# Performance work log

Hardware: AMD Instinct MI355X
Metric: run time of the kernel (lower is better)

The kernel has to match this reference:

```python
import jax, jax.numpy as jnp
import numpy as np

B, V, H, W, CIN, COUT = 2, 4, 256, 256, 64, 64
WINDOW = 1
GAMMA = 0.1


def setup_inputs() -> dict:
    key = jax.random.key(0)
    ks = jax.random.split(key, 6)
    # gaussian positions: x,y in [-1,1], z in [0.5,2.5] so projection masks are nontrivial
    means = jax.random.uniform(ks[0], (B, V, H, W, 3), dtype=jnp.float32)
    means = means * jnp.array([2.0, 2.0, 2.0], jnp.float32) + jnp.array([-1.0, -1.0, 0.5], jnp.float32)
    depths = jax.random.uniform(ks[1], (B, V, H, W, 1, 1), dtype=jnp.float32)
    gs_feats = jax.random.normal(ks[2], (B, V, H, W, CIN), dtype=jnp.float32)
    # normalized intrinsics (ndc in [0,1))
    intr = jnp.array([[0.8, 0.0, 0.5], [0.0, 0.8, 0.5], [0.0, 0.0, 1.0]], jnp.float32)
    intrinsics = jnp.broadcast_to(intr, (B, V, 3, 3))
    # camera-to-world extrinsics: identity rotation, small per-view translations
    t = jax.random.uniform(ks[3], (B, V, 3), minval=-0.2, maxval=0.2, dtype=jnp.float32)
    extrinsics = jnp.broadcast_to(jnp.eye(4, dtype=jnp.float32), (B, V, 4, 4)).at[..., :3, 3].set(t)
    w1 = jax.random.normal(ks[4], (COUT, CIN, 3, 3), dtype=jnp.float32) * 0.05
    b1 = jnp.zeros((COUT,), jnp.float32)
    w2 = jax.random.normal(ks[5], (COUT, COUT, 3, 3), dtype=jnp.float32) * 0.05
    b2 = jnp.zeros((COUT,), jnp.float32)
    return {"means": means, "depths": depths, "gs_feats": gs_feats,
            "intrinsics": intrinsics, "extrinsics": extrinsics,
            "w1": w1, "b1": b1, "w2": w2, "b2": b2}


def _project(points, intr, extr, eps=1e-8):
    # points (b, n, 3) world; extr (b,4,4) cam-to-world; intr (b,3,3) normalized
    w2c = jnp.linalg.inv(extr)
    ph = jnp.concatenate([points, jnp.ones_like(points[..., :1])], axis=-1)  # (b,n,4)
    cam = jnp.einsum('bij,bnj->bni', w2c, ph)[..., :3]
    z = cam[..., 2:3]
    ndc = jnp.einsum('bij,bnj->bni', intr, cam / (z + eps))
    return ndc[..., :2], cam[..., 2] > eps


def _conv3x3(x, w, b):
    y = jax.lax.conv_general_dilated(x, w, (1, 1), 'SAME',
                                     dimension_numbers=('NCHW', 'OIHW', 'NCHW'))
    return y + b[None, :, None, None]


def reference(means, depths, gs_feats, intrinsics, extrinsics, w1, b1, w2, b2):
    b, v, h, w_, c = gs_feats.shape
    hw = h * w_
    feats_flat = gs_feats.reshape(b, v, hw, c)
    pts = means.reshape(b, v, hw, 3)
    outs = []
    for j in range(v):
        acc = feats_flat[:, j]                      # (b, hw, c)
        norm = jnp.ones((b,), gs_feats.dtype)
        for k in range(v):
            if j != k and (k - WINDOW) <= j <= (k + WINDOW):
                ndc, valid_z = _project(pts[:, j], intrinsics[:, k], extrinsics[:, k])
                px = jnp.floor(ndc[..., 0] * w_).astype(jnp.int32)
                py = jnp.floor(ndc[..., 1] * h).astype(jnp.int32)
                mask = ((ndc[..., 0] >= 0) & (ndc[..., 0] < 1) &
                        (ndc[..., 1] >= 0) & (ndc[..., 1] < 1) & valid_z)  # (b,hw)
                idx = jnp.clip(py, 0, h - 1) * w_ + jnp.clip(px, 0, w_ - 1)
                gathered = jnp.take_along_axis(feats_flat[:, k], idx[..., None], axis=1)
                upd = jnp.where(mask[..., None], gathered, jnp.zeros((), gs_feats.dtype))
                scale = GAMMA * mask.sum(-1).astype(gs_feats.dtype) / (h * w_)  # (b,)
                acc = acc + upd * scale[:, None, None]
                norm = norm + scale
        outs.append(acc / norm[:, None, None])
    fused = jnp.stack(outs, axis=1).reshape(b * v, h, w_, c).transpose(0, 3, 1, 2)  # (bv,c,h,w)
    x = _conv3x3(fused, w1, b1)
    x = jax.nn.gelu(x, approximate=False)
    x = _conv3x3(x, w2, b2)
    return x.transpose(0, 2, 3, 1).reshape(b, v, h, w_, -1)
```

## Files before the change

kernel.cpp:

```cpp
#include <hip/hip_runtime.h>
#include <math.h>

#define HW 65536
#define NPAD 258

typedef short bf16x8 __attribute__((ext_vector_type(8)));
typedef float f32x4  __attribute__((ext_vector_type(4)));

#define O_COUNTS 0
#define O_W2C    2048
#define O_WT     4096
#define O_META   151552
#define O_FUSED  3297280
#define O_X1     71458816

#define ROWPX 66
#define ROWB  (ROWPX * 128)
#define ROWSTR (ROWB + 16)
#define ROWSTRS (ROWSTR / 2)

__device__ __forceinline__ unsigned short f2bf(float f) {
    unsigned int u = __float_as_uint(f);
    u += 0x7FFFu + ((u >> 16) & 1u);
    return (unsigned short)(u >> 16);
}

__global__ __launch_bounds__(256) void prep_kernel(
    const float* __restrict__ extr, const float* __restrict__ w1,
    const float* __restrict__ w2, float* __restrict__ w2c,
    unsigned short* __restrict__ wT, unsigned short* __restrict__ fusedP,
    unsigned short* __restrict__ x1P, int* __restrict__ counts)
{
    int tid = blockIdx.x * blockDim.x + threadIdx.x;
    int nth = gridDim.x * blockDim.x;

    if (blockIdx.x == 0) {
        if (threadIdx.x < 8) {
            float a[4][8];
            const float* E = extr + threadIdx.x * 16;
            for (int r = 0; r < 4; r++)
                for (int c = 0; c < 4; c++) {
                    a[r][c] = E[r*4 + c];
                    a[r][4+c] = (r == c) ? 1.0f : 0.0f;
                }
            for (int col = 0; col < 4; col++) {
                int piv = col; float bm = fabsf(a[col][col]);
                for (int r = col+1; r < 4; r++) {
                    float v = fabsf(a[r][col]);
                    if (v > bm) { bm = v; piv = r; }
                }
                if (piv != col)
                    for (int c = 0; c < 8; c++) { float t = a[col][c]; a[col][c] = a[piv][c]; a[piv][c] = t; }
                float f = 1.0f / a[col][col];
                for (int c = 0; c < 8; c++) a[col][c] *= f;
                for (int r = 0; r < 4; r++) if (r != col) {
                    float f2 = a[r][col];
                    for (int c = 0; c < 8; c++) a[r][c] -= f2 * a[col][c];
                }
            }
            float* O = w2c + threadIdx.x * 16;
            for (int r = 0; r < 4; r++)
                for (int c = 0; c < 4; c++) O[r*4+c] = a[r][4+c];
        }
    }

    for (int i = tid; i < 384; i += nth) counts[i] = 0;

    for (int e = tid; e < 73728; e += nth) {
        int t = e;
        int j  = t & 7;  t >>= 3;
        int co = t & 63; t >>= 6;
        int q  = t & 3;  t >>= 2;
        int tap = t % 9; t /= 9;
        int h  = t & 1;  int cv = t >> 1;
        int ci = h*32 + q*8 + j;
        int ky = tap / 3, kx = tap % 3;
        const float* wsrc = cv ? w2 : w1;
        float v = wsrc[((co*64 + ci)*3 + ky)*3 + kx];
        wT[cv*36864 + ((((h*9 + tap)*4 + q)*64 + co)*8 + j)] = f2bf(v);
    }

    for (int u = tid; u < 2*8*1028*8; u += nth) {
        int t = u;
        int ch   = t & 7;    t >>= 3;
        int cell = t % 1028; t /= 1028;
        int n    = t & 7;    int buf = t >> 3;
        int y, x;
        if      (cell < 258) { y = 0;   x = cell; }
        else if (cell < 516) { y = 257; x = cell - 258; }
        else if (cell < 772) { y = cell - 516 + 1; x = 0; }
        else                 { y = cell - 772 + 1; x = 257; }
        unsigned short* p = (buf ? x1P : fusedP) +
            (((size_t)(n*NPAD + y)*NPAD + x)*64 + ch*8);
        *reinterpret_cast<uint4*>(p) = make_uint4(0u, 0u, 0u, 0u);
    }
}

__global__ __launch_bounds__(256) void proj_kernel(
    const float* __restrict__ means, const float* __restrict__ intr,
    const float* __restrict__ w2c, int* __restrict__ meta,
    int* __restrict__ counts)
{
    const int jt[6] = {0,1,1,2,2,3};
    const int kt[6] = {1,0,2,1,3,2};
    int s = blockIdx.y;
    int b = s / 6, p = s % 6;
    int j = jt[p], k = kt[p];
    int i = blockIdx.x * 256 + threadIdx.x;

    __shared__ int bcnt;
    if (threadIdx.x == 0) bcnt = 0;
    __syncthreads();

    const float* mp = means + ((size_t)(b*4 + j)*HW + i)*3;
    float x = mp[0], y = mp[1], z = mp[2];
    const float* M = w2c + (b*4 + k)*16;
    const float* I = intr + (b*4 + k)*9;

    float cx = fmaf(M[2],  z, fmaf(M[1], y, M[0]*x)) + M[3];
    float cy = fmaf(M[6],  z, fmaf(M[5], y, M[4]*x)) + M[7];
    float cz = fmaf(M[10], z, fmaf(M[9], y, M[8]*x)) + M[11];

    bool vz = cz > 1e-8f;
    float zi = cz + 1e-8f;
    float sx = cx / zi, sy = cy / zi, sz = cz / zi;
    float nx = fmaf(I[2], sz, fmaf(I[1], sy, I[0]*sx));
    float ny = fmaf(I[5], sz, fmaf(I[4], sy, I[3]*sx));

    int px = (int)floorf(nx * 256.0f);
    int py = (int)floorf(ny * 256.0f);
    bool mask = (nx >= 0.0f) && (nx < 1.0f) && (ny >= 0.0f) && (ny < 1.0f) && vz;
    int pxc = min(max(px, 0), 255);
    int pyc = min(max(py, 0), 255);
    int idx = pyc*256 + pxc;
    meta[(size_t)s*HW + i] = idx | (mask ? (int)0x80000000 : 0);

    unsigned long long bal = __ballot(mask ? 1 : 0);
    if ((threadIdx.x & 63) == 0)
        atomicAdd(&bcnt, (int)__popcll(bal));
    __syncthreads();
    if (threadIdx.x == 0)
        atomicAdd(counts + s*32, bcnt);
}

__global__ __launch_bounds__(256) void fuse_kernel(
    const float* __restrict__ feats, const int* __restrict__ meta,
    const int* __restrict__ counts, unsigned short* __restrict__ fusedP)
{
    const int nsl[4]    = {1, 2, 2, 1};
    const int slt[4][2] = {{0,0},{1,2},{3,4},{5,5}};
    const int kvw[4][2] = {{1,1},{0,2},{1,3},{2,2}};

    int bj = blockIdx.y;
    int b = bj >> 2, j = bj & 3;
    int pt = blockIdx.x * 16 + (threadIdx.x >> 4);
    int cg = threadIdx.x & 15;

    const float4* fj = reinterpret_cast<const float4*>(
        feats + ((size_t)bj*HW + pt)*64) + cg;
    float4 acc = *fj;
    float norm = 1.0f;
    int ns = nsl[j];
    for (int e = 0; e < 2; e++) {
        if (e < ns) {
            int p = slt[j][e], k = kvw[j][e];
            int s = b*6 + p;
            float scale = 0.1f * (float)counts[s*32] / 65536.0f;
            int mt = meta[(size_t)s*HW + pt];
            if (mt < 0) {
                int idx = mt & 0xFFFF;
                const float4* g = reinterpret_cast<const float4*>(
                    feats + ((size_t)(b*4 + k)*HW + idx)*64) + cg;
                float4 gv = *g;
                acc.x += scale * gv.x; acc.y += scale * gv.y;
                acc.z += scale * gv.z; acc.w += scale * gv.w;
            }
            norm += scale;
        }
    }
    float ox = acc.x / norm, oy = acc.y / norm;
    float oz = acc.z / norm, ow = acc.w / norm;

    int yy = pt >> 8, xx = pt & 255;
    unsigned short* op = fusedP +
        (((size_t)bj*NPAD + (yy+1))*NPAD + (xx+1))*64 + cg*4;
    ushort4 o = make_ushort4(f2bf(ox), f2bf(oy), f2bf(oz), f2bf(ow));
    *reinterpret_cast<ushort4*>(op) = o;
}

template<int MODE>
__global__ __launch_bounds__(256) void conv_kernel(
    const unsigned short* __restrict__ in, const unsigned short* __restrict__ wT,
    const float* __restrict__ bias, void* __restrict__ outp)
{
    __shared__ unsigned short smem[6 * ROWSTRS];

    int n = blockIdx.z;
    int y0 = blockIdx.y * 4;
    int X0 = blockIdx.x * 64;
    int w  = threadIdx.x >> 6;
    int lane = threadIdx.x & 63;
    int m = lane & 15, q = lane >> 4;

    for (int ri = w; ri < 6; ri += 4) {
        const char* g = (const char*)(in + ((size_t)(n*NPAD + y0 + ri)*NPAD + X0)*64);
        char* l = (char*)smem + ri*ROWSTR;
#pragma unroll
        for (int i = 0; i < 8; i++)
            __builtin_amdgcn_global_load_lds(
                (const __attribute__((address_space(1))) unsigned int*)(g + i*1024 + (size_t)lane*16),
                (__attribute__((address_space(3))) unsigned int*)(l + i*1024 + (size_t)lane*16),
                16, 0, 0);
        __builtin_amdgcn_global_load_lds(
            (const __attribute__((address_space(1))) unsigned int*)(g + 8192 + (size_t)lane*4),
            (__attribute__((address_space(3))) unsigned int*)(l + 8192 + (size_t)lane*4),
            4, 0, 0);
    }
    __syncthreads();

    f32x4 acc[4][4];
#pragma unroll
    for (int a = 0; a < 4; a++)
#pragma unroll
        for (int bq = 0; bq < 4; bq++)
            acc[a][bq] = (f32x4){0.f, 0.f, 0.f, 0.f};

#pragma unroll
    for (int h = 0; h < 2; h++) {
#pragma unroll
        for (int tap = 0; tap < 9; tap++) {
            int dy = tap/3, dx = tap%3;
            const unsigned short* lrow = smem + (w + dy)*ROWSTRS;
            bf16x8 av[4], bv[4];
#pragma unroll
            for (int Mt = 0; Mt < 4; Mt++)
                av[Mt] = *reinterpret_cast<const bf16x8*>(
                    lrow + (Mt*16 + m + dx)*64 + h*32 + q*8);
            const unsigned short* wp = wT + (size_t)(((h*9 + tap)*4 + q)*64)*8;
#pragma unroll
            for (int Nt = 0; Nt < 4; Nt++)
                bv[Nt] = *reinterpret_cast<const bf16x8*>(wp + (Nt*16 + m)*8);
#pragma unroll
            for (int Mt = 0; Mt < 4; Mt++)
#pragma unroll
                for (int Nt = 0; Nt < 4; Nt++)
                    acc[Mt][Nt] = __builtin_amdgcn_mfma_f32_16x16x32_bf16(
                        av[Mt], bv[Nt], acc[Mt][Nt], 0, 0, 0);
        }
    }

#pragma unroll
    for (int Nt = 0; Nt < 4; Nt++) {
        int co = Nt*16 + m;
        float bs = bias[co];
#pragma unroll
        for (int Mt = 0; Mt < 4; Mt++) {
#pragma unroll
            for (int r = 0; r < 4; r++) {
                float v = acc[Mt][Nt][r] + bs;
                int px = X0 + Mt*16 + q*4 + r;
                if (MODE == 1) {
                    v = 0.5f * v * (1.0f + erff(v * 0.70710678118654752f));
                    unsigned short* o = (unsigned short*)outp +
                        ((size_t)(n*NPAD + y0 + w + 1)*NPAD + (px + 1))*64 + co;
                    *o = f2bf(v);
                } else {
                    float* o = (float*)outp +
                        ((size_t)(n*256 + y0 + w)*256 + px)*64 + co;
                    *o = v;
                }
            }
        }
    }
}

extern "C" void kernel_launch(void* const* d_in, const int* in_sizes, int n_in,
                              void* d_out, int out_size, void* d_ws, size_t ws_size,
                              hipStream_t stream)
{
    const float* means = (const float*)d_in[0];
    const float* feats = (const float*)d_in[2];
    const float* intr  = (const float*)d_in[3];
    const float* extr  = (const float*)d_in[4];
    const float* w1    = (const float*)d_in[5];
    const float* b1    = (const float*)d_in[6];
    const float* w2    = (const float*)d_in[7];
    const float* b2    = (const float*)d_in[8];

    char* ws = (char*)d_ws;
    int*            counts = (int*)(ws + O_COUNTS);
    float*          w2c    = (float*)(ws + O_W2C);
    unsigned short* wT     = (unsigned short*)(ws + O_WT);
    int*            meta   = (int*)(ws + O_META);
    unsigned short* fusedP = (unsigned short*)(ws + O_FUSED);
    unsigned short* x1P    = (unsigned short*)(ws + O_X1);

    prep_kernel<<<dim3(96), dim3(256), 0, stream>>>(
        extr, w1, w2, w2c, wT, fusedP, x1P, counts);
    proj_kernel<<<dim3(256, 12), dim3(256), 0, stream>>>(
        means, intr, w2c, meta, counts);
    fuse_kernel<<<dim3(4096, 8), dim3(256), 0, stream>>>(
        feats, meta, counts, fusedP);
    conv_kernel<1><<<dim3(4, 64, 8), dim3(256), 0, stream>>>(
        fusedP, wT, b1, (void*)x1P);
    conv_kernel<2><<<dim3(4, 64, 8), dim3(256), 0, stream>>>(
        x1P, wT + 36864, b2, d_out);
}
```

Before: 417.5 us.

## Swizzle conv LDS tile layout and vectorize epilogue stores via swapped MFMA operands

Conv input rows are now staged into LDS with an XOR swizzle on the 16-byte channel chunks, and the A-fragment reads use matching swizzled offsets. This is meant to remove LDS bank conflicts when lanes read neighbouring pixels. The MFMA operands are swapped so each lane holds four consecutive output channels, which lets the epilogue load bias as float4 and write packed ushort4/float4 stores instead of scalar ones. The swizzle must agree exactly between the load and read paths, including the 2-pixel tail loaded with 4-byte copies.

```diff
diff --git a/kernel.cpp b/kernel.cpp
--- a/kernel.cpp
+++ b/kernel.cpp
@@ -202,22 +202,37 @@
     int lane = threadIdx.x & 63;
     int m = lane & 15, q = lane >> 4;
 
+    int sub = lane >> 3;
+    int ch8 = lane & 7;
+    int srcoff = sub*128 + (((ch8 ^ sub) & 7) << 4);
+    int tpx = lane >> 5;
+    int tch = (lane >> 2) & 7;
+    int tsrc = 8192 + tpx*128 + ((((tch ^ tpx) & 7)) << 4) + (lane & 3)*4;
+
     for (int ri = w; ri < 6; ri += 4) {
         const char* g = (const char*)(in + ((size_t)(n*NPAD + y0 + ri)*NPAD + X0)*64);
         char* l = (char*)smem + ri*ROWSTR;
 #pragma unroll
         for (int i = 0; i < 8; i++)
             __builtin_amdgcn_global_load_lds(
-                (const __attribute__((address_space(1))) unsigned int*)(g + i*1024 + (size_t)lane*16),
+                (const __attribute__((address_space(1))) unsigned int*)(g + i*1024 + srcoff),
                 (__attribute__((address_space(3))) unsigned int*)(l + i*1024 + (size_t)lane*16),
                 16, 0, 0);
         __builtin_amdgcn_global_load_lds(
-            (const __attribute__((address_space(1))) unsigned int*)(g + 8192 + (size_t)lane*4),
+            (const __attribute__((address_space(1))) unsigned int*)(g + tsrc),
             (__attribute__((address_space(3))) unsigned int*)(l + 8192 + (size_t)lane*4),
             4, 0, 0);
     }
     __syncthreads();
 
+    int rowb = w * ROWSTR;
+    int vb[2][3];
+#pragma unroll
+    for (int h = 0; h < 2; h++)
+#pragma unroll
+        for (int dx = 0; dx < 3; dx++)
+            vb[h][dx] = rowb + m*128 + ((((h*4 + q) ^ ((m + dx) & 7)) & 7) << 4);
+
     f32x4 acc[4][4];
 #pragma unroll
     for (int a = 0; a < 4; a++)
@@ -230,12 +245,11 @@
 #pragma unroll
         for (int tap = 0; tap < 9; tap++) {
             int dy = tap/3, dx = tap%3;
-            const unsigned short* lrow = smem + (w + dy)*ROWSTRS;
             bf16x8 av[4], bv[4];
 #pragma unroll
             for (int Mt = 0; Mt < 4; Mt++)
                 av[Mt] = *reinterpret_cast<const bf16x8*>(
-                    lrow + (Mt*16 + m + dx)*64 + h*32 + q*8);
+                    (const char*)smem + vb[h][dx] + dy*ROWSTR + (Mt*16 + dx)*128);
             const unsigned short* wp = wT + (size_t)(((h*9 + tap)*4 + q)*64)*8;
 #pragma unroll
             for (int Nt = 0; Nt < 4; Nt++)
@@ -245,30 +259,38 @@
 #pragma unroll
                 for (int Nt = 0; Nt < 4; Nt++)
                     acc[Mt][Nt] = __builtin_amdgcn_mfma_f32_16x16x32_bf16(
-                        av[Mt], bv[Nt], acc[Mt][Nt], 0, 0, 0);
+                        bv[Nt], av[Mt], acc[Mt][Nt], 0, 0, 0);
         }
     }
 
-#pragma unroll
-    for (int Nt = 0; Nt < 4; Nt++) {
-        int co = Nt*16 + m;
-        float bs = bias[co];
-#pragma unroll
-        for (int Mt = 0; Mt < 4; Mt++) {
-#pragma unroll
-            for (int r = 0; r < 4; r++) {
-                float v = acc[Mt][Nt][r] + bs;
-                int px = X0 + Mt*16 + q*4 + r;
-                if (MODE == 1) {
-                    v = 0.5f * v * (1.0f + erff(v * 0.70710678118654752f));
-                    unsigned short* o = (unsigned short*)outp +
-                        ((size_t)(n*NPAD + y0 + w + 1)*NPAD + (px + 1))*64 + co;
-                    *o = f2bf(v);
-                } else {
-                    float* o = (float*)outp +
-                        ((size_t)(n*256 + y0 + w)*256 + px)*64 + co;
-                    *o = v;
-                }
+    float4 bsv[4];
+#pragma unroll
+    for (int Nt = 0; Nt < 4; Nt++)
+        bsv[Nt] = *reinterpret_cast<const float4*>(bias + Nt*16 + q*4);
+
+#pragma unroll
+    for (int Mt = 0; Mt < 4; Mt++) {
+        int px = X0 + Mt*16 + m;
+#pragma unroll
+        for (int Nt = 0; Nt < 4; Nt++) {
+            int co0 = Nt*16 + q*4;
+            float v0 = acc[Mt][Nt][0] + bsv[Nt].x;
+            float v1 = acc[Mt][Nt][1] + bsv[Nt].y;
+            float v2 = acc[Mt][Nt][2] + bsv[Nt].z;
+            float v3 = acc[Mt][Nt][3] + bsv[Nt].w;
+            if (MODE == 1) {
+                v0 = 0.5f * v0 * (1.0f + erff(v0 * 0.70710678118654752f));
+                v1 = 0.5f * v1 * (1.0f + erff(v1 * 0.70710678118654752f));
+                v2 = 0.5f * v2 * (1.0f + erff(v2 * 0.70710678118654752f));
+                v3 = 0.5f * v3 * (1.0f + erff(v3 * 0.70710678118654752f));
+                unsigned short* o = (unsigned short*)outp +
+                    ((size_t)(n*NPAD + y0 + w + 1)*NPAD + (px + 1))*64 + co0;
+                ushort4 pk = make_ushort4(f2bf(v0), f2bf(v1), f2bf(v2), f2bf(v3));
+                *reinterpret_cast<ushort4*>(o) = pk;
+            } else {
+                float* o = (float*)outp +
+                    ((size_t)(n*256 + y0 + w)*256 + px)*64 + co0;
+                *reinterpret_cast<float4*>(o) = make_float4(v0, v1, v2, v3);
             }
         }
     }
```

Result: faster. 397.7 us (-4.8%).
